# Performance work log

Measured on AMD Instinct MI355X. Metric: run time of the kernel, lower is better.

The kernel has to match this reference:

```python
import jax, jax.numpy as jnp
import numpy as np

B, A, DIN, HID, HEADS, NOUT, K = 256, 64, 64, 128, 4, 2, 7
N = B * A                      # 16384 nodes
C = HID                        # per-head dim == out_channels (module quirk)
SCALE = (HID // HEADS) ** -0.5 # 1/sqrt(32), as in the module


def _xavier(k, shape):
    fan_out, fan_in = shape
    lim = (6.0 / (fan_in + fan_out)) ** 0.5
    return jax.random.uniform(k, shape, jnp.float32, -lim, lim)


def setup_inputs() -> dict:
    key = jax.random.key(0)
    ks = jax.random.split(key, 24)
    x = jax.random.normal(ks[0], (N, DIN), jnp.float32)
    pos_b = jax.random.uniform(ks[1], (B, A, 2), jnp.float32) * 10.0  # [B,A,2]
    pos = pos_b.reshape(N, 2)

    # kNN graph per environment (replicates torch.cdist + topk smallest, drop self)
    d = jnp.linalg.norm(pos_b[:, :, None, :] - pos_b[:, None, :, :], axis=-1)  # [B,A,A]
    _, idx = jax.lax.top_k(-d, K + 1)
    nb = idx[..., 1:]                                   # [B,A,K] neighbor ids
    offs = (jnp.arange(B) * A)[:, None, None]
    src = jnp.broadcast_to(jnp.arange(A)[None, :, None], (B, A, K)) + offs
    dst = nb + offs
    loops = jnp.arange(N)
    edge_index = jnp.stack([
        jnp.concatenate([src.reshape(-1), loops]),
        jnp.concatenate([dst.reshape(-1), loops]),
    ]).astype(jnp.int32)                                # [2, E], E = B*A*K + N

    inp = {"x": x, "pos": pos, "edge_index": edge_index}
    inp["l0_Wq"] = _xavier(ks[2], (HEADS * C, 2))
    inp["l0_Wk"] = _xavier(ks[3], (HEADS * C, 2))
    inp["l0_Wv"] = _xavier(ks[4], (HEADS * C, DIN))
    inp["l0_Wo"] = _xavier(ks[5], (HID, HEADS * C))
    inp["l0_bo"] = jnp.zeros((HID,), jnp.float32)
    inp["l1_Wq"] = _xavier(ks[6], (HEADS * C, 2))
    inp["l1_Wk"] = _xavier(ks[7], (HEADS * C, 2))
    inp["l1_Wv"] = _xavier(ks[8], (HEADS * C, HID))
    inp["l1_Wo"] = _xavier(ks[9], (HID, HEADS * C))
    inp["l1_bo"] = jnp.zeros((HID,), jnp.float32)
    inp["W1"] = _xavier(ks[10], (256, HID))
    inp["b1"] = jnp.zeros((256,), jnp.float32)
    inp["W2"] = _xavier(ks[11], (256, 256))
    inp["b2"] = jnp.zeros((256,), jnp.float32)
    inp["W3"] = _xavier(ks[12], (NOUT, 256))
    inp["b3"] = jnp.zeros((NOUT,), jnp.float32)
    return inp


def _gat(x, pos, src, dst, Wq, Wk, Wv, Wo, bo):
    # positions -> Q/K, features -> V (position-aware attention)
    q = (pos @ Wq.T).reshape(N, HEADS, C)
    k = (pos @ Wk.T).reshape(N, HEADS, C)
    v = (x @ Wv.T).reshape(N, HEADS, C)
    # per-edge logits, segment softmax over incoming edges of dst
    alpha = jnp.einsum('ehc,ehc->eh', q[dst], k[src]) * SCALE        # [E,H]
    amax = jax.ops.segment_max(alpha, dst, num_segments=N)           # [N,H]
    ex = jnp.exp(alpha - amax[dst])
    a = ex / jax.ops.segment_sum(ex, dst, num_segments=N)[dst]
    msg = v[src] * a[..., None]                                      # [E,H,C]
    agg = jax.ops.segment_sum(msg, dst, num_segments=N)              # [N,H,C]
    return agg.reshape(N, HEADS * C) @ Wo.T + bo


def reference(x, pos, edge_index,
              l0_Wq, l0_Wk, l0_Wv, l0_Wo, l0_bo,
              l1_Wq, l1_Wk, l1_Wv, l1_Wo, l1_bo,
              W1, b1, W2, b2, W3, b3):
    src, dst = edge_index[0], edge_index[1]
    h = jnp.tanh(_gat(x, pos, src, dst, l0_Wq, l0_Wk, l0_Wv, l0_Wo, l0_bo))
    h = jnp.tanh(_gat(h, pos, src, dst, l1_Wq, l1_Wk, l1_Wv, l1_Wo, l1_bo))
    h = jax.nn.relu(h @ W1.T + b1)
    h = jax.nn.relu(h @ W2.T + b2)
    out = h @ W3.T + b3
    return out.reshape(B, A, NOUT)
```

## Files before the change

kernel.cpp:

```cpp
#include <hip/hip_runtime.h>
#include <hip/hip_bf16.h>
#include <cstddef>
#include <math.h>

#define N_NODES 16384
#define DIN 64
#define HID 128
#define SCALE_F 0.17677669529663687f

using bf16x8 = __attribute__((ext_vector_type(8))) short;
using f32x4  = __attribute__((ext_vector_type(4))) float;

__device__ __forceinline__ ushort f2b(float x) {
  __hip_bfloat16 h = __float2bfloat16(x);
  return *(ushort*)&h;
}
__device__ __forceinline__ float b2f(ushort u) {
  __hip_bfloat16 h = *(__hip_bfloat16*)&u;
  return __bfloat162float(h);
}
__device__ __forceinline__ void split1(float x, ushort& h, ushort& l) {
  h = f2b(x);
  l = f2b(x - b2f(h));
}
__device__ __forceinline__ void split3(float x, ushort& a, ushort& b, ushort& c) {
  a = f2b(x);
  float r1 = x - b2f(a);
  b = f2b(r1);
  c = f2b(r1 - b2f(b));
}

#define MFMA(d, A, B) d = __builtin_amdgcn_mfma_f32_16x16x32_bf16(A, B, d, 0, 0, 0)


__global__ __launch_bounds__(256) void prep_all_kernel(
    const float* __restrict__ Wq0, const float* __restrict__ Wk0,
    const float* __restrict__ Wq1, const float* __restrict__ Wk1,
    float* __restrict__ G,
    const float* __restrict__ Wv0, const float* __restrict__ Wo0,
    ushort* __restrict__ M0a, ushort* __restrict__ M0b, ushort* __restrict__ M0c,
    const float* __restrict__ Wv1, const float* __restrict__ Wo1,
    ushort* __restrict__ M1a, ushort* __restrict__ M1b, ushort* __restrict__ M1c,
    const float* __restrict__ W1, ushort* __restrict__ W1hi, ushort* __restrict__ W1lo,
    const float* __restrict__ W2, ushort* __restrict__ W2hi, ushort* __restrict__ W2lo,
    unsigned long long* __restrict__ out64)
{
  int blk = blockIdx.x, t = threadIdx.x;
  if (blk == 0) {
    if (t >= 32) return;
    int l = t >> 4, h = (t >> 2) & 3, a = (t >> 1) & 1, b = t & 1;
    const float* Wq = l ? Wq1 : Wq0;
    const float* Wk = l ? Wk1 : Wk0;
    float acc = 0.f;
    for (int c = 0; c < 128; c++)
      acc += Wq[(h * 128 + c) * 2 + a] * Wk[(h * 128 + c) * 2 + b];
    G[t] = acc;
  } else if (blk < 385) {
    int D, idx;
    const float *Wv, *Wo;
    ushort *Ma, *Mb, *Mc;
    if (blk < 129) { D = DIN; idx = (blk - 1) * 256 + t; Wv = Wv0; Wo = Wo0; Ma = M0a; Mb = M0b; Mc = M0c; }
    else           { D = HID; idx = (blk - 129) * 256 + t; Wv = Wv1; Wo = Wo1; Ma = M1a; Mb = M1b; Mc = M1c; }
    int K4 = 4 * D;
    int o = idx / K4, hd = idx - o * K4;
    int h = hd / D, d = hd - h * D;
    const float* wv = Wv + (size_t)(h * 128) * D + d;
    const float* wo = Wo + (size_t)o * 512 + h * 128;
    float acc = 0.f;
    for (int c = 0; c < 128; c++)
      acc += wv[(size_t)c * D] * wo[c];
    split3(acc, Ma[idx], Mb[idx], Mc[idx]);
  } else if (blk < 769) {
    int i = (blk - 385) * 256 + t;
    if (i < 256 * 128) split1(W1[i], W1hi[i], W1lo[i]);
    int j = i - 256 * 128;
    if (j >= 0 && j < 256 * 256) split1(W2[j], W2hi[j], W2lo[j]);
  } else {
    int i = (blk - 769) * 256 + t;
    if (i < N_NODES) out64[i] = 0ull;
  }
}


#define PF 136

#define AFRAG_OFF 26624
#define LDS_USHORTS 59392

template <int KD>
__device__ __forceinline__ void gat_layer(
    int wave, int lane, int lm, int lq,
    const ushort* sFa, const ushort* sFb, const ushort* sFc,
    ushort* aA,
    const float* psx, const float* psy,
    const float* pdx, const float* pdy,
    const unsigned long long* m64,
    const float* __restrict__ G,
    const ushort* __restrict__ Ma, const ushort* __restrict__ Mb,
    const ushort* __restrict__ Mc,
    f32x4 hacc[4])
{
  {
    int wm = wave & 3;
    float pdxm = (wm & 2) ? ((wm & 1) ? pdx[3] : pdx[2]) : ((wm & 1) ? pdx[1] : pdx[0]);
    float pdym = (wm & 2) ? ((wm & 1) ? pdy[3] : pdy[2]) : ((wm & 1) ? pdy[1] : pdy[0]);
    unsigned long long mm = (wm & 2) ? ((wm & 1) ? m64[3] : m64[2])
                                     : ((wm & 1) ? m64[1] : m64[0]);
    unsigned mb0 = (unsigned)((mm >> (8 * lq)) & 0xFF);
    unsigned mb1 = (unsigned)((mm >> (32 + 8 * lq)) & 0xFF);
#pragma unroll
    for (int pi = 0; pi < 2; pi++) {
      int h = (wave >> 2) + 2 * pi;
      float g0 = G[h * 4], g1 = G[h * 4 + 1], g2 = G[h * 4 + 2], g3 = G[h * 4 + 3];
      float a0 = (g0 * pdxm + g2 * pdym) * SCALE_F;
      float a1 = (g1 * pdxm + g3 * pdym) * SCALE_F;
      float sshift = a0 * pdxm + a1 * pdym;
      float e[16];
      float sum = 0.f;
#pragma unroll
      for (int j = 0; j < 8; j++) {
        e[j]     = ((mb0 >> j) & 1) ? __expf(a0 * psx[j] + a1 * psy[j] - sshift) : 0.f;
        e[8 + j] = ((mb1 >> j) & 1) ? __expf(a0 * psx[8 + j] + a1 * psy[8 + j] - sshift) : 0.f;
        sum += e[j] + e[8 + j];
      }
      sum += __shfl_xor(sum, 16);
      sum += __shfl_xor(sum, 32);
      float inv = 1.f / sum;
      bf16x8 Aa0, Aa1, Ab0, Ab1;
#pragma unroll
      for (int j = 0; j < 8; j++) {
        ushort ua, ub;
        split1(e[j] * inv, ua, ub);     Aa0[j] = (short)ua; Ab0[j] = (short)ub;
        split1(e[8 + j] * inv, ua, ub); Aa1[j] = (short)ua; Ab1[j] = (short)ub;
      }
      int sbase = (h * 4 + wm) * 2048 + lane * 8;
      *(bf16x8*)&aA[sbase]        = Aa0;
      *(bf16x8*)&aA[sbase + 512]  = Aa1;
      *(bf16x8*)&aA[sbase + 1024] = Ab0;
      *(bf16x8*)&aA[sbase + 1536] = Ab1;
    }
  }
  __syncthreads();

  const int K4 = 4 * KD;
  const int o = 16 * wave + lm;
#pragma unroll
  for (int i = 0; i < 4; i++) hacc[i] = (f32x4){0.f, 0.f, 0.f, 0.f};

#pragma unroll 1
  for (int h = 0; h < 4; h++) {
    f32x4 y[4];
#pragma unroll
    for (int i = 0; i < 4; i++) y[i] = (f32x4){0.f, 0.f, 0.f, 0.f};
#pragma unroll 1
    for (int kf = 0; kf < KD / 32; kf++) {
      size_t boff = (size_t)o * K4 + h * KD + kf * 32 + lq * 8;
      bf16x8 ma = *(const bf16x8*)&Ma[boff];
      bf16x8 mb = *(const bf16x8*)&Mb[boff];
      bf16x8 mc = *(const bf16x8*)&Mc[boff];
#pragma unroll
      for (int mp = 0; mp < 2; mp++) {
        int f0 = (mp * 32 + lm) * PF + kf * 32 + lq * 8;
        int f1 = (mp * 32 + 16 + lm) * PF + kf * 32 + lq * 8;
        bf16x8 fa0 = *(const bf16x8*)&sFa[f0], fa1 = *(const bf16x8*)&sFa[f1];
        bf16x8 fb0 = *(const bf16x8*)&sFb[f0], fb1 = *(const bf16x8*)&sFb[f1];
        bf16x8 fc0 = *(const bf16x8*)&sFc[f0], fc1 = *(const bf16x8*)&sFc[f1];
        f32x4 y0 = y[mp * 2], y1 = y[mp * 2 + 1];
        MFMA(y0, fa0, ma); MFMA(y1, fa1, ma);
        MFMA(y0, fa0, mb); MFMA(y1, fa1, mb);
        MFMA(y0, fb0, ma); MFMA(y1, fb1, ma);
        MFMA(y0, fa0, mc); MFMA(y1, fa1, mc);
        MFMA(y0, fc0, ma); MFMA(y1, fc1, ma);
        MFMA(y0, fb0, mb); MFMA(y1, fb1, mb);
        y[mp * 2] = y0; y[mp * 2 + 1] = y1;
      }
    }
    bf16x8 Ya[2], Yb[2];
#pragma unroll
    for (int kb = 0; kb < 2; kb++) {
#pragma unroll
      for (int j = 0; j < 8; j++) {
        int sl = ((2 * lq + (j >> 2)) & 3) * 16 + lm;
        float v0 = __shfl(y[2 * kb][j & 3], sl);
        float v1 = __shfl(y[2 * kb + 1][j & 3], sl);
        float v = (lq & 2) ? v1 : v0;
        ushort ua, ub;
        split1(v, ua, ub);
        Ya[kb][j] = (short)ua; Yb[kb][j] = (short)ub;
      }
    }
#pragma unroll
    for (int mtd = 0; mtd < 4; mtd++) {
      int abase = (h * 4 + mtd) * 2048 + lane * 8;
      bf16x8 Aa0 = *(const bf16x8*)&aA[abase];
      bf16x8 Aa1 = *(const bf16x8*)&aA[abase + 512];
      bf16x8 Ab0 = *(const bf16x8*)&aA[abase + 1024];
      bf16x8 Ab1 = *(const bf16x8*)&aA[abase + 1536];
      MFMA(hacc[mtd], Aa0, Ya[0]);
      MFMA(hacc[mtd], Aa0, Yb[0]);
      MFMA(hacc[mtd], Ab0, Ya[0]);
      MFMA(hacc[mtd], Ab0, Yb[0]);
      MFMA(hacc[mtd], Aa1, Ya[1]);
      MFMA(hacc[mtd], Aa1, Yb[1]);
      MFMA(hacc[mtd], Ab1, Ya[1]);
      MFMA(hacc[mtd], Ab1, Yb[1]);
    }
  }
}

__global__ __attribute__((amdgpu_flat_work_group_size(512, 512), amdgpu_waves_per_eu(2)))
void fused_gat_kernel(
    const float* __restrict__ x, const float* __restrict__ pos,
    const int* __restrict__ srcp, const int* __restrict__ dstp,
    const float* __restrict__ G,
    const ushort* __restrict__ M0a, const ushort* __restrict__ M0b, const ushort* __restrict__ M0c,
    const ushort* __restrict__ M1a, const ushort* __restrict__ M1b, const ushort* __restrict__ M1c,
    const float* __restrict__ bo0, const float* __restrict__ bo1,
    const ushort* __restrict__ W1hi, const ushort* __restrict__ W1lo, const float* __restrict__ b1,
    const ushort* __restrict__ W2hi, const ushort* __restrict__ W2lo, const float* __restrict__ b2,
    const float* __restrict__ W3, const float* __restrict__ b3,
    float* __restrict__ outp)
{
  __shared__ __align__(16) ushort uBig[LDS_USHORTS];
  ushort* sFa = uBig;
  ushort* sFb = uBig + 8704;
  ushort* sFc = uBig + 17408;
  float* pxs = (float*)(uBig + 26112);
  float* pys = (float*)(uBig + 26240);
  unsigned long long* smask = (unsigned long long*)(uBig + 26368);
  ushort* aA = uBig + AFRAG_OFF;
  ushort* pA = uBig + AFRAG_OFF;
  ushort* pB = uBig + AFRAG_OFF + 16384;

  int b = blockIdx.x, t = threadIdx.x;
  int wave = t >> 6, lane = t & 63, lm = lane & 15, lq = lane >> 4;

  if (t < 64) {
    pxs[t] = pos[(b * 64 + t) * 2];
    pys[t] = pos[(b * 64 + t) * 2 + 1];
    smask[t] = 1ull << t;
  }
  {
    const float4* gx = (const float4*)(x + (size_t)b * 64 * DIN);
#pragma unroll
    for (int i = 0; i < 2; i++) {
      int idx = t + i * 512;
      float4 v = gx[idx];
      int r = idx >> 4, c = (idx & 15) * 4;
      ushort4 ua, ub, uc;
      split3(v.x, ua.x, ub.x, uc.x); split3(v.y, ua.y, ub.y, uc.y);
      split3(v.z, ua.z, ub.z, uc.z); split3(v.w, ua.w, ub.w, uc.w);
      *(ushort4*)&sFa[r * PF + c] = ua;
      *(ushort4*)&sFb[r * PF + c] = ub;
      *(ushort4*)&sFc[r * PF + c] = uc;
    }
  }
  __syncthreads();
  if (t < 448) {
    int s = srcp[b * 448 + t];
    int d = dstp[b * 448 + t];
    atomicOr(&smask[d & 63], 1ull << (s & 63));
  }
  __syncthreads();
  unsigned long long m64[4];
#pragma unroll
  for (int mtd = 0; mtd < 4; mtd++) m64[mtd] = smask[mtd * 16 + lm];

  float psx[16], psy[16], pdx[4], pdy[4];
#pragma unroll
  for (int j = 0; j < 8; j++) {
    psx[j] = pxs[8 * lq + j];          psy[j] = pys[8 * lq + j];
    psx[8 + j] = pxs[32 + 8 * lq + j]; psy[8 + j] = pys[32 + 8 * lq + j];
  }
#pragma unroll
  for (int mtd = 0; mtd < 4; mtd++) {
    pdx[mtd] = pxs[mtd * 16 + lm];
    pdy[mtd] = pys[mtd * 16 + lm];
  }

  f32x4 hacc[4];
  gat_layer<DIN>(wave, lane, lm, lq, sFa, sFb, sFc, aA, psx, psy, pdx, pdy, m64,
                 G, M0a, M0b, M0c, hacc);
  __syncthreads();
  int o = 16 * wave + lm;
  {
    float bv = bo0[o];
#pragma unroll
    for (int mtd = 0; mtd < 4; mtd++)
#pragma unroll
      for (int r = 0; r < 4; r++) {
        int dst = mtd * 16 + lq * 4 + r;
        ushort ua, ub, uc;
        split3(tanhf(hacc[mtd][r] + bv), ua, ub, uc);
        sFa[dst * PF + o] = ua;
        sFb[dst * PF + o] = ub;
        sFc[dst * PF + o] = uc;
      }
  }
  __syncthreads();
  gat_layer<HID>(wave, lane, lm, lq, sFa, sFb, sFc, aA, psx, psy, pdx, pdy, m64,
                 G + 16, M1a, M1b, M1c, hacc);
  float h2v[4][4];
  {
    float bv = bo1[o];
#pragma unroll
    for (int mtd = 0; mtd < 4; mtd++)
#pragma unroll
      for (int r = 0; r < 4; r++)
        h2v[mtd][r] = tanhf(hacc[mtd][r] + bv);
  }
  __syncthreads();
#pragma unroll
  for (int mtd = 0; mtd < 4; mtd++)
#pragma unroll
    for (int r = 0; r < 4; r++) {
      int dst = mtd * 16 + lq * 4 + r;
      ushort hh, ll;
      split1(h2v[mtd][r], hh, ll);
      sFa[dst * PF + o] = hh;
      sFb[dst * PF + o] = ll;
    }
  __syncthreads();
  f32x4 y1[2][4];
#pragma unroll
  for (int ti = 0; ti < 2; ti++)
#pragma unroll
    for (int mtd = 0; mtd < 4; mtd++) y1[ti][mtd] = (f32x4){0.f, 0.f, 0.f, 0.f};
#pragma unroll 1
  for (int kf = 0; kf < 4; kf++) {
    int ko = kf * 32 + lq * 8;
    bf16x8 bh0 = *(const bf16x8*)&W1hi[(size_t)(32 * wave + lm) * 128 + ko];
    bf16x8 bl0 = *(const bf16x8*)&W1lo[(size_t)(32 * wave + lm) * 128 + ko];
    bf16x8 bh1 = *(const bf16x8*)&W1hi[(size_t)(32 * wave + 16 + lm) * 128 + ko];
    bf16x8 bl1 = *(const bf16x8*)&W1lo[(size_t)(32 * wave + 16 + lm) * 128 + ko];
#pragma unroll
    for (int mtd = 0; mtd < 4; mtd++) {
      bf16x8 ah = *(const bf16x8*)&sFa[(mtd * 16 + lm) * PF + ko];
      bf16x8 al = *(const bf16x8*)&sFb[(mtd * 16 + lm) * PF + ko];
      MFMA(y1[0][mtd], ah, bh0);
      MFMA(y1[0][mtd], ah, bl0);
      MFMA(y1[0][mtd], al, bh0);
      MFMA(y1[1][mtd], ah, bh1);
      MFMA(y1[1][mtd], ah, bl1);
      MFMA(y1[1][mtd], al, bh1);
    }
  }
#pragma unroll
  for (int ti = 0; ti < 2; ti++) {
    int col = 32 * wave + ti * 16 + lm;
    float bv = b1[col];
#pragma unroll
    for (int mtd = 0; mtd < 4; mtd++)
#pragma unroll
      for (int r = 0; r < 4; r++) {
        int row = mtd * 16 + lq * 4 + r;
        float v = fmaxf(y1[ti][mtd][r] + bv, 0.f);
        ushort hh, ll;
        split1(v, hh, ll);
        int cc = col ^ ((row & 15) << 3);
        pA[row * 256 + cc] = hh;
        pB[row * 256 + cc] = ll;
      }
  }
  __syncthreads();
  f32x4 y2[2][4];
#pragma unroll
  for (int ti = 0; ti < 2; ti++)
#pragma unroll
    for (int mtd = 0; mtd < 4; mtd++) y2[ti][mtd] = (f32x4){0.f, 0.f, 0.f, 0.f};
#pragma unroll 1
  for (int kf = 0; kf < 8; kf++) {
    int ko = kf * 32 + lq * 8;
    bf16x8 bh0 = *(const bf16x8*)&W2hi[(size_t)(32 * wave + lm) * 256 + ko];
    bf16x8 bl0 = *(const bf16x8*)&W2lo[(size_t)(32 * wave + lm) * 256 + ko];
    bf16x8 bh1 = *(const bf16x8*)&W2hi[(size_t)(32 * wave + 16 + lm) * 256 + ko];
    bf16x8 bl1 = *(const bf16x8*)&W2lo[(size_t)(32 * wave + 16 + lm) * 256 + ko];
#pragma unroll
    for (int mtd = 0; mtd < 4; mtd++) {
      int row = mtd * 16 + lm;
      int cc = ko ^ ((row & 15) << 3);
      bf16x8 ah = *(const bf16x8*)&pA[row * 256 + cc];
      bf16x8 al = *(const bf16x8*)&pB[row * 256 + cc];
      MFMA(y2[0][mtd], ah, bh0);
      MFMA(y2[0][mtd], ah, bl0);
      MFMA(y2[0][mtd], al, bh0);
      MFMA(y2[1][mtd], ah, bh1);
      MFMA(y2[1][mtd], ah, bl1);
      MFMA(y2[1][mtd], al, bh1);
    }
  }
  {
    int c0 = 32 * wave + lm, c1 = c0 + 16;
    float w300 = W3[c0], w301 = W3[c1];
    float w310 = W3[256 + c0], w311 = W3[256 + c1];
    float b20 = b2[c0], b21 = b2[c1];
    float bb0 = (wave == 0) ? b3[0] : 0.f;
    float bb1 = (wave == 0) ? b3[1] : 0.f;
#pragma unroll
    for (int mtd = 0; mtd < 4; mtd++)
#pragma unroll
      for (int r = 0; r < 4; r++) {
        float va = fmaxf(y2[0][mtd][r] + b20, 0.f);
        float vb = fmaxf(y2[1][mtd][r] + b21, 0.f);
        float s0 = va * w300 + vb * w301;
        float s1 = va * w310 + vb * w311;
        s0 += __shfl_xor(s0, 1); s0 += __shfl_xor(s0, 2);
        s0 += __shfl_xor(s0, 4); s0 += __shfl_xor(s0, 8);
        s1 += __shfl_xor(s1, 1); s1 += __shfl_xor(s1, 2);
        s1 += __shfl_xor(s1, 4); s1 += __shfl_xor(s1, 8);
        if (lm == 0) {
          int row = b * 64 + mtd * 16 + lq * 4 + r;
          atomicAdd(&outp[row * 2 + 0], s0 + bb0);
          atomicAdd(&outp[row * 2 + 1], s1 + bb1);
        }
      }
  }
}


extern "C" void kernel_launch(void* const* d_in, const int* in_sizes, int n_in,
                              void* d_out, int out_size, void* d_ws, size_t ws_size,
                              hipStream_t stream) {
  const float* x     = (const float*)d_in[0];
  const float* pos   = (const float*)d_in[1];
  const int*   ei    = (const int*)d_in[2];
  const float* l0_Wq = (const float*)d_in[3];
  const float* l0_Wk = (const float*)d_in[4];
  const float* l0_Wv = (const float*)d_in[5];
  const float* l0_Wo = (const float*)d_in[6];
  const float* l0_bo = (const float*)d_in[7];
  const float* l1_Wq = (const float*)d_in[8];
  const float* l1_Wk = (const float*)d_in[9];
  const float* l1_Wv = (const float*)d_in[10];
  const float* l1_Wo = (const float*)d_in[11];
  const float* l1_bo = (const float*)d_in[12];
  const float* W1    = (const float*)d_in[13];
  const float* b1    = (const float*)d_in[14];
  const float* W2    = (const float*)d_in[15];
  const float* b2    = (const float*)d_in[16];
  const float* W3    = (const float*)d_in[17];
  const float* b3    = (const float*)d_in[18];
  float* outp = (float*)d_out;

  int E = in_sizes[2] / 2;
  const int* srcp = ei;
  const int* dstp = ei + E;

  char* base = (char*)d_ws;
  size_t off = 0;
  auto alloc = [&](size_t bytes) -> void* {
    void* p = base + off;
    off = (off + bytes + 255) & ~(size_t)255;
    return p;
  };
  float*  G   = (float*)alloc(32 * sizeof(float));
  ushort* M0a = (ushort*)alloc((size_t)128 * 256 * 2);
  ushort* M0b = (ushort*)alloc((size_t)128 * 256 * 2);
  ushort* M0c = (ushort*)alloc((size_t)128 * 256 * 2);
  ushort* M1a = (ushort*)alloc((size_t)128 * 512 * 2);
  ushort* M1b = (ushort*)alloc((size_t)128 * 512 * 2);
  ushort* M1c = (ushort*)alloc((size_t)128 * 512 * 2);
  ushort* W1hi = (ushort*)alloc((size_t)256 * 128 * 2);
  ushort* W1lo = (ushort*)alloc((size_t)256 * 128 * 2);
  ushort* W2hi = (ushort*)alloc((size_t)256 * 256 * 2);
  ushort* W2lo = (ushort*)alloc((size_t)256 * 256 * 2);

  prep_all_kernel<<<833, 256, 0, stream>>>(
      l0_Wq, l0_Wk, l1_Wq, l1_Wk, G,
      l0_Wv, l0_Wo, M0a, M0b, M0c,
      l1_Wv, l1_Wo, M1a, M1b, M1c,
      W1, W1hi, W1lo, W2, W2hi, W2lo,
      (unsigned long long*)outp);

  fused_gat_kernel<<<N_NODES / 64, 512, 0, stream>>>(
      x, pos, srcp, dstp, G, M0a, M0b, M0c, M1a, M1b, M1c, l0_bo, l1_bo,
      W1hi, W1lo, b1, W2hi, W2lo, b2, W3, b3, outp);

  (void)n_in; (void)out_size; (void)ws_size;
}
```

Before: 160.0 us.

## Double block to 1024 threads, split heads across waves, swizzle LDS feature layout

Doubles the fused kernel's workgroup to 16 waves. Each wave now computes attention for one head and quarter, and the output tile's head loop is split between two wave groups whose partial results are combined through a new LDS buffer. The padded feature rows (PF=136) are replaced by an XOR-swizzled 128-wide layout to save LDS and avoid bank conflicts. The MLP tiles shrink to 16 columns per wave. The goal is more parallelism and latency hiding per block. The cost is more LDS per block (about 150KB), an extra reduction and sync, and lower per-wave reuse of B fragments.

```diff
diff --git a/kernel.cpp b/kernel.cpp
--- a/kernel.cpp
+++ b/kernel.cpp
@@ -82,19 +82,22 @@
 }
 
 
-#define PF 136
-
-#define AFRAG_OFF 26624
-#define LDS_USHORTS 59392
+#define SFB_OFF 8192
+#define SFC_OFF 16384
+#define PXS_OFF 24576
+#define PYS_OFF 24704
+#define SMASK_OFF 24832
+#define AFRAG_OFF 25088
+#define PH_OFF 57856
+#define LDS_USHORTS 74752
 
 template <int KD>
 __device__ __forceinline__ void gat_layer(
     int wave, int lane, int lm, int lq,
     const ushort* sFa, const ushort* sFb, const ushort* sFc,
     ushort* aA,
-    const float* psx, const float* psy,
-    const float* pdx, const float* pdy,
-    const unsigned long long* m64,
+    const float* pxs, const float* pys,
+    const unsigned long long* smask,
     const float* __restrict__ G,
     const ushort* __restrict__ Ma, const ushort* __restrict__ Mb,
     const ushort* __restrict__ Mc,
@@ -102,53 +105,51 @@
 {
   {
     int wm = wave & 3;
-    float pdxm = (wm & 2) ? ((wm & 1) ? pdx[3] : pdx[2]) : ((wm & 1) ? pdx[1] : pdx[0]);
-    float pdym = (wm & 2) ? ((wm & 1) ? pdy[3] : pdy[2]) : ((wm & 1) ? pdy[1] : pdy[0]);
-    unsigned long long mm = (wm & 2) ? ((wm & 1) ? m64[3] : m64[2])
-                                     : ((wm & 1) ? m64[1] : m64[0]);
+    int h = wave >> 2;
+    float pdxm = pxs[wm * 16 + lm];
+    float pdym = pys[wm * 16 + lm];
+    unsigned long long mm = smask[wm * 16 + lm];
     unsigned mb0 = (unsigned)((mm >> (8 * lq)) & 0xFF);
     unsigned mb1 = (unsigned)((mm >> (32 + 8 * lq)) & 0xFF);
-#pragma unroll
-    for (int pi = 0; pi < 2; pi++) {
-      int h = (wave >> 2) + 2 * pi;
-      float g0 = G[h * 4], g1 = G[h * 4 + 1], g2 = G[h * 4 + 2], g3 = G[h * 4 + 3];
-      float a0 = (g0 * pdxm + g2 * pdym) * SCALE_F;
-      float a1 = (g1 * pdxm + g3 * pdym) * SCALE_F;
-      float sshift = a0 * pdxm + a1 * pdym;
-      float e[16];
-      float sum = 0.f;
-#pragma unroll
-      for (int j = 0; j < 8; j++) {
-        e[j]     = ((mb0 >> j) & 1) ? __expf(a0 * psx[j] + a1 * psy[j] - sshift) : 0.f;
-        e[8 + j] = ((mb1 >> j) & 1) ? __expf(a0 * psx[8 + j] + a1 * psy[8 + j] - sshift) : 0.f;
-        sum += e[j] + e[8 + j];
-      }
-      sum += __shfl_xor(sum, 16);
-      sum += __shfl_xor(sum, 32);
-      float inv = 1.f / sum;
-      bf16x8 Aa0, Aa1, Ab0, Ab1;
-#pragma unroll
-      for (int j = 0; j < 8; j++) {
-        ushort ua, ub;
-        split1(e[j] * inv, ua, ub);     Aa0[j] = (short)ua; Ab0[j] = (short)ub;
-        split1(e[8 + j] * inv, ua, ub); Aa1[j] = (short)ua; Ab1[j] = (short)ub;
-      }
-      int sbase = (h * 4 + wm) * 2048 + lane * 8;
-      *(bf16x8*)&aA[sbase]        = Aa0;
-      *(bf16x8*)&aA[sbase + 512]  = Aa1;
-      *(bf16x8*)&aA[sbase + 1024] = Ab0;
-      *(bf16x8*)&aA[sbase + 1536] = Ab1;
-    }
+    float g0 = G[h * 4], g1 = G[h * 4 + 1], g2 = G[h * 4 + 2], g3 = G[h * 4 + 3];
+    float a0 = (g0 * pdxm + g2 * pdym) * SCALE_F;
+    float a1 = (g1 * pdxm + g3 * pdym) * SCALE_F;
+    float sshift = a0 * pdxm + a1 * pdym;
+    float e[16];
+    float sum = 0.f;
+#pragma unroll
+    for (int j = 0; j < 8; j++) {
+      e[j]     = ((mb0 >> j) & 1) ? __expf(a0 * pxs[8 * lq + j] + a1 * pys[8 * lq + j] - sshift) : 0.f;
+      e[8 + j] = ((mb1 >> j) & 1) ? __expf(a0 * pxs[32 + 8 * lq + j] + a1 * pys[32 + 8 * lq + j] - sshift) : 0.f;
+      sum += e[j] + e[8 + j];
+    }
+    sum += __shfl_xor(sum, 16);
+    sum += __shfl_xor(sum, 32);
+    float inv = 1.f / sum;
+    bf16x8 Aa0, Aa1, Ab0, Ab1;
+#pragma unroll
+    for (int j = 0; j < 8; j++) {
+      ushort ua, ub;
+      split1(e[j] * inv, ua, ub);     Aa0[j] = (short)ua; Ab0[j] = (short)ub;
+      split1(e[8 + j] * inv, ua, ub); Aa1[j] = (short)ua; Ab1[j] = (short)ub;
+    }
+    int sbase = wave * 2048 + lane * 8;
+    *(bf16x8*)&aA[sbase]        = Aa0;
+    *(bf16x8*)&aA[sbase + 512]  = Aa1;
+    *(bf16x8*)&aA[sbase + 1024] = Ab0;
+    *(bf16x8*)&aA[sbase + 1536] = Ab1;
   }
   __syncthreads();
 
   const int K4 = 4 * KD;
-  const int o = 16 * wave + lm;
+  const int o = 16 * (wave & 7) + lm;
+  const int hb = wave >> 3;
 #pragma unroll
   for (int i = 0; i < 4; i++) hacc[i] = (f32x4){0.f, 0.f, 0.f, 0.f};
 
 #pragma unroll 1
-  for (int h = 0; h < 4; h++) {
+  for (int hi = 0; hi < 2; hi++) {
+    int h = 2 * hb + hi;
     f32x4 y[4];
 #pragma unroll
     for (int i = 0; i < 4; i++) y[i] = (f32x4){0.f, 0.f, 0.f, 0.f};
@@ -158,10 +159,12 @@
       bf16x8 ma = *(const bf16x8*)&Ma[boff];
       bf16x8 mb = *(const bf16x8*)&Mb[boff];
       bf16x8 mc = *(const bf16x8*)&Mc[boff];
+      int ko = kf * 32 + lq * 8;
+      int sw = lm << 3;
 #pragma unroll
       for (int mp = 0; mp < 2; mp++) {
-        int f0 = (mp * 32 + lm) * PF + kf * 32 + lq * 8;
-        int f1 = (mp * 32 + 16 + lm) * PF + kf * 32 + lq * 8;
+        int f0 = (mp * 32 + lm) * 128 + (ko ^ sw);
+        int f1 = f0 + 16 * 128;
         bf16x8 fa0 = *(const bf16x8*)&sFa[f0], fa1 = *(const bf16x8*)&sFa[f1];
         bf16x8 fb0 = *(const bf16x8*)&sFb[f0], fb1 = *(const bf16x8*)&sFb[f1];
         bf16x8 fc0 = *(const bf16x8*)&sFc[f0], fc1 = *(const bf16x8*)&sFc[f1];
@@ -208,7 +211,7 @@
   }
 }
 
-__global__ __attribute__((amdgpu_flat_work_group_size(512, 512), amdgpu_waves_per_eu(2)))
+__global__ __attribute__((amdgpu_flat_work_group_size(1024, 1024), amdgpu_waves_per_eu(4)))
 void fused_gat_kernel(
     const float* __restrict__ x, const float* __restrict__ pos,
     const int* __restrict__ srcp, const int* __restrict__ dstp,
@@ -223,14 +226,15 @@
 {
   __shared__ __align__(16) ushort uBig[LDS_USHORTS];
   ushort* sFa = uBig;
-  ushort* sFb = uBig + 8704;
-  ushort* sFc = uBig + 17408;
-  float* pxs = (float*)(uBig + 26112);
-  float* pys = (float*)(uBig + 26240);
-  unsigned long long* smask = (unsigned long long*)(uBig + 26368);
+  ushort* sFb = uBig + SFB_OFF;
+  ushort* sFc = uBig + SFC_OFF;
+  float* pxs = (float*)(uBig + PXS_OFF);
+  float* pys = (float*)(uBig + PYS_OFF);
+  unsigned long long* smask = (unsigned long long*)(uBig + SMASK_OFF);
   ushort* aA = uBig + AFRAG_OFF;
   ushort* pA = uBig + AFRAG_OFF;
   ushort* pB = uBig + AFRAG_OFF + 16384;
+  float* pH = (float*)(uBig + PH_OFF);
 
   int b = blockIdx.x, t = threadIdx.x;
   int wave = t >> 6, lane = t & 63, lm = lane & 15, lq = lane >> 4;
@@ -242,18 +246,15 @@
   }
   {
     const float4* gx = (const float4*)(x + (size_t)b * 64 * DIN);
-#pragma unroll
-    for (int i = 0; i < 2; i++) {
-      int idx = t + i * 512;
-      float4 v = gx[idx];
-      int r = idx >> 4, c = (idx & 15) * 4;
-      ushort4 ua, ub, uc;
-      split3(v.x, ua.x, ub.x, uc.x); split3(v.y, ua.y, ub.y, uc.y);
-      split3(v.z, ua.z, ub.z, uc.z); split3(v.w, ua.w, ub.w, uc.w);
-      *(ushort4*)&sFa[r * PF + c] = ua;
-      *(ushort4*)&sFb[r * PF + c] = ub;
-      *(ushort4*)&sFc[r * PF + c] = uc;
-    }
+    float4 v = gx[t];
+    int r = t >> 4, c = (t & 15) * 4;
+    int cs = c ^ ((r & 15) << 3);
+    ushort4 ua, ub, uc;
+    split3(v.x, ua.x, ub.x, uc.x); split3(v.y, ua.y, ub.y, uc.y);
+    split3(v.z, ua.z, ub.z, uc.z); split3(v.w, ua.w, ub.w, uc.w);
+    *(ushort4*)&sFa[r * 128 + cs] = ua;
+    *(ushort4*)&sFb[r * 128 + cs] = ub;
+    *(ushort4*)&sFc[r * 128 + cs] = uc;
   }
   __syncthreads();
   if (t < 448) {
@@ -262,99 +263,91 @@
     atomicOr(&smask[d & 63], 1ull << (s & 63));
   }
   __syncthreads();
-  unsigned long long m64[4];
-#pragma unroll
-  for (int mtd = 0; mtd < 4; mtd++) m64[mtd] = smask[mtd * 16 + lm];
-
-  float psx[16], psy[16], pdx[4], pdy[4];
-#pragma unroll
-  for (int j = 0; j < 8; j++) {
-    psx[j] = pxs[8 * lq + j];          psy[j] = pys[8 * lq + j];
-    psx[8 + j] = pxs[32 + 8 * lq + j]; psy[8 + j] = pys[32 + 8 * lq + j];
-  }
-#pragma unroll
-  for (int mtd = 0; mtd < 4; mtd++) {
-    pdx[mtd] = pxs[mtd * 16 + lm];
-    pdy[mtd] = pys[mtd * 16 + lm];
-  }
 
   f32x4 hacc[4];
-  gat_layer<DIN>(wave, lane, lm, lq, sFa, sFb, sFc, aA, psx, psy, pdx, pdy, m64,
+  gat_layer<DIN>(wave, lane, lm, lq, sFa, sFb, sFc, aA, pxs, pys, smask,
                  G, M0a, M0b, M0c, hacc);
-  __syncthreads();
-  int o = 16 * wave + lm;
-  {
+  int o = 16 * (wave & 7) + lm;
+  if (wave >= 8) {
+#pragma unroll
+    for (int mtd = 0; mtd < 4; mtd++)
+#pragma unroll
+      for (int r = 0; r < 4; r++)
+        pH[(mtd * 16 + lq * 4 + r) * 132 + o] = hacc[mtd][r];
+  }
+  __syncthreads();
+  if (wave < 8) {
     float bv = bo0[o];
 #pragma unroll
     for (int mtd = 0; mtd < 4; mtd++)
 #pragma unroll
       for (int r = 0; r < 4; r++) {
         int dst = mtd * 16 + lq * 4 + r;
+        float v = tanhf(hacc[mtd][r] + pH[dst * 132 + o] + bv);
         ushort ua, ub, uc;
-        split3(tanhf(hacc[mtd][r] + bv), ua, ub, uc);
-        sFa[dst * PF + o] = ua;
-        sFb[dst * PF + o] = ub;
-        sFc[dst * PF + o] = uc;
-      }
-  }
-  __syncthreads();
-  gat_layer<HID>(wave, lane, lm, lq, sFa, sFb, sFc, aA, psx, psy, pdx, pdy, m64,
+        split3(v, ua, ub, uc);
+        int cs = o ^ ((dst & 15) << 3);
+        sFa[dst * 128 + cs] = ua;
+        sFb[dst * 128 + cs] = ub;
+        sFc[dst * 128 + cs] = uc;
+      }
+  }
+  __syncthreads();
+  gat_layer<HID>(wave, lane, lm, lq, sFa, sFb, sFc, aA, pxs, pys, smask,
                  G + 16, M1a, M1b, M1c, hacc);
-  float h2v[4][4];
-  {
+  if (wave >= 8) {
+#pragma unroll
+    for (int mtd = 0; mtd < 4; mtd++)
+#pragma unroll
+      for (int r = 0; r < 4; r++)
+        pH[(mtd * 16 + lq * 4 + r) * 132 + o] = hacc[mtd][r];
+  }
+  __syncthreads();
+  if (wave < 8) {
     float bv = bo1[o];
 #pragma unroll
     for (int mtd = 0; mtd < 4; mtd++)
 #pragma unroll
-      for (int r = 0; r < 4; r++)
-        h2v[mtd][r] = tanhf(hacc[mtd][r] + bv);
-  }
-  __syncthreads();
-#pragma unroll
-  for (int mtd = 0; mtd < 4; mtd++)
-#pragma unroll
-    for (int r = 0; r < 4; r++) {
-      int dst = mtd * 16 + lq * 4 + r;
-      ushort hh, ll;
-      split1(h2v[mtd][r], hh, ll);
-      sFa[dst * PF + o] = hh;
-      sFb[dst * PF + o] = ll;
-    }
-  __syncthreads();
-  f32x4 y1[2][4];
-#pragma unroll
-  for (int ti = 0; ti < 2; ti++)
-#pragma unroll
-    for (int mtd = 0; mtd < 4; mtd++) y1[ti][mtd] = (f32x4){0.f, 0.f, 0.f, 0.f};
+      for (int r = 0; r < 4; r++) {
+        int dst = mtd * 16 + lq * 4 + r;
+        float v = tanhf(hacc[mtd][r] + pH[dst * 132 + o] + bv);
+        ushort hh, ll;
+        split1(v, hh, ll);
+        int cs = o ^ ((dst & 15) << 3);
+        sFa[dst * 128 + cs] = hh;
+        sFb[dst * 128 + cs] = ll;
+      }
+  }
+  __syncthreads();
+  f32x4 y1[4];
+#pragma unroll
+  for (int mtd = 0; mtd < 4; mtd++) y1[mtd] = (f32x4){0.f, 0.f, 0.f, 0.f};
 #pragma unroll 1
   for (int kf = 0; kf < 4; kf++) {
     int ko = kf * 32 + lq * 8;
-    bf16x8 bh0 = *(const bf16x8*)&W1hi[(size_t)(32 * wave + lm) * 128 + ko];
-    bf16x8 bl0 = *(const bf16x8*)&W1lo[(size_t)(32 * wave + lm) * 128 + ko];
-    bf16x8 bh1 = *(const bf16x8*)&W1hi[(size_t)(32 * wave + 16 + lm) * 128 + ko];
-    bf16x8 bl1 = *(const bf16x8*)&W1lo[(size_t)(32 * wave + 16 + lm) * 128 + ko];
+    int col = 16 * wave + lm;
+    bf16x8 bh = *(const bf16x8*)&W1hi[(size_t)col * 128 + ko];
+    bf16x8 bl = *(const bf16x8*)&W1lo[(size_t)col * 128 + ko];
 #pragma unroll
     for (int mtd = 0; mtd < 4; mtd++) {
-      bf16x8 ah = *(const bf16x8*)&sFa[(mtd * 16 + lm) * PF + ko];
-      bf16x8 al = *(const bf16x8*)&sFb[(mtd * 16 + lm) * PF + ko];
-      MFMA(y1[0][mtd], ah, bh0);
-      MFMA(y1[0][mtd], ah, bl0);
-      MFMA(y1[0][mtd], al, bh0);
-      MFMA(y1[1][mtd], ah, bh1);
-      MFMA(y1[1][mtd], ah, bl1);
-      MFMA(y1[1][mtd], al, bh1);
-    }
-  }
-#pragma unroll
-  for (int ti = 0; ti < 2; ti++) {
-    int col = 32 * wave + ti * 16 + lm;
+      int row = mtd * 16 + lm;
+      int cs = ko ^ (lm << 3);
+      bf16x8 ah = *(const bf16x8*)&sFa[row * 128 + cs];
+      bf16x8 al = *(const bf16x8*)&sFb[row * 128 + cs];
+      MFMA(y1[mtd], ah, bh);
+      MFMA(y1[mtd], ah, bl);
+      MFMA(y1[mtd], al, bh);
+    }
+  }
+  {
+    int col = 16 * wave + lm;
     float bv = b1[col];
 #pragma unroll
     for (int mtd = 0; mtd < 4; mtd++)
 #pragma unroll
       for (int r = 0; r < 4; r++) {
         int row = mtd * 16 + lq * 4 + r;
-        float v = fmaxf(y1[ti][mtd][r] + bv, 0.f);
+        float v = fmaxf(y1[mtd][r] + bv, 0.f);
         ushort hh, ll;
         split1(v, hh, ll);
         int cc = col ^ ((row & 15) << 3);
@@ -363,47 +356,38 @@
       }
   }
   __syncthreads();
-  f32x4 y2[2][4];
-#pragma unroll
-  for (int ti = 0; ti < 2; ti++)
-#pragma unroll
-    for (int mtd = 0; mtd < 4; mtd++) y2[ti][mtd] = (f32x4){0.f, 0.f, 0.f, 0.f};
+  f32x4 y2[4];
+#pragma unroll
+  for (int mtd = 0; mtd < 4; mtd++) y2[mtd] = (f32x4){0.f, 0.f, 0.f, 0.f};
 #pragma unroll 1
   for (int kf = 0; kf < 8; kf++) {
     int ko = kf * 32 + lq * 8;
-    bf16x8 bh0 = *(const bf16x8*)&W2hi[(size_t)(32 * wave + lm) * 256 + ko];
-    bf16x8 bl0 = *(const bf16x8*)&W2lo[(size_t)(32 * wave + lm) * 256 + ko];
-    bf16x8 bh1 = *(const bf16x8*)&W2hi[(size_t)(32 * wave + 16 + lm) * 256 + ko];
-    bf16x8 bl1 = *(const bf16x8*)&W2lo[(size_t)(32 * wave + 16 + lm) * 256 + ko];
+    bf16x8 bh = *(const bf16x8*)&W2hi[(size_t)(16 * wave + lm) * 256 + ko];
+    bf16x8 bl = *(const bf16x8*)&W2lo[(size_t)(16 * wave + lm) * 256 + ko];
 #pragma unroll
     for (int mtd = 0; mtd < 4; mtd++) {
       int row = mtd * 16 + lm;
-      int cc = ko ^ ((row & 15) << 3);
+      int cc = ko ^ (lm << 3);
       bf16x8 ah = *(const bf16x8*)&pA[row * 256 + cc];
       bf16x8 al = *(const bf16x8*)&pB[row * 256 + cc];
-      MFMA(y2[0][mtd], ah, bh0);
-      MFMA(y2[0][mtd], ah, bl0);
-      MFMA(y2[0][mtd], al, bh0);
-      MFMA(y2[1][mtd], ah, bh1);
-      MFMA(y2[1][mtd], ah, bl1);
-      MFMA(y2[1][mtd], al, bh1);
+      MFMA(y2[mtd], ah, bh);
+      MFMA(y2[mtd], ah, bl);
+      MFMA(y2[mtd], al, bh);
     }
   }
   {
-    int c0 = 32 * wave + lm, c1 = c0 + 16;
-    float w300 = W3[c0], w301 = W3[c1];
-    float w310 = W3[256 + c0], w311 = W3[256 + c1];
-    float b20 = b2[c0], b21 = b2[c1];
+    int c0 = 16 * wave + lm;
+    float w30 = W3[c0], w31 = W3[256 + c0];
+    float b20 = b2[c0];
     float bb0 = (wave == 0) ? b3[0] : 0.f;
     float bb1 = (wave == 0) ? b3[1] : 0.f;
 #pragma unroll
     for (int mtd = 0; mtd < 4; mtd++)
 #pragma unroll
       for (int r = 0; r < 4; r++) {
-        float va = fmaxf(y2[0][mtd][r] + b20, 0.f);
-        float vb = fmaxf(y2[1][mtd][r] + b21, 0.f);
-        float s0 = va * w300 + vb * w301;
-        float s1 = va * w310 + vb * w311;
+        float va = fmaxf(y2[mtd][r] + b20, 0.f);
+        float s0 = va * w30;
+        float s1 = va * w31;
         s0 += __shfl_xor(s0, 1); s0 += __shfl_xor(s0, 2);
         s0 += __shfl_xor(s0, 4); s0 += __shfl_xor(s0, 8);
         s1 += __shfl_xor(s1, 1); s1 += __shfl_xor(s1, 2);
@@ -472,7 +456,7 @@
       W1, W1hi, W1lo, W2, W2hi, W2lo,
       (unsigned long long*)outp);
 
-  fused_gat_kernel<<<N_NODES / 64, 512, 0, stream>>>(
+  fused_gat_kernel<<<N_NODES / 64, 1024, 0, stream>>>(
       x, pos, srcp, dstp, G, M0a, M0b, M0c, M1a, M1b, M1c, l0_bo, l1_bo,
       W1hi, W1lo, b1, W2hi, W2lo, b2, W3, b3, outp);
 
```

After: 151.7 us. 5.2% less time.
